# Performance work log

Hardware: AMD Instinct MI355X
Metric: run time of the kernel (lower is better)

The kernel has to match this reference:

```python
import jax, jax.numpy as jnp
import numpy as np

HEADS = 4
DIM_HEAD = 32
EPS = 1e-5


def setup_inputs() -> dict:
    key = jax.random.key(0)
    ks = jax.random.split(key, 3)
    b, c, h, w = 32, 256, 64, 64
    hidden = HEADS * DIM_HEAD  # 128
    x = jax.random.normal(ks[0], (b, c, h, w), dtype=jnp.float32)
    w_qkv = jax.random.normal(ks[1], (3 * hidden, c), dtype=jnp.float32) * 0.02
    w_out = jax.random.normal(ks[2], (c, hidden), dtype=jnp.float32) * 0.02
    b_out = jnp.zeros((c,), dtype=jnp.float32)
    gn_w = jnp.ones((c,), dtype=jnp.float32)
    gn_b = jnp.zeros((c,), dtype=jnp.float32)
    return {"x": x, "w_qkv": w_qkv, "w_out": w_out, "b_out": b_out,
            "gn_w": gn_w, "gn_b": gn_b}


def reference(x, w_qkv, w_out, b_out, gn_w, gn_b):
    b, c, h, w = x.shape
    n = h * w
    scale = DIM_HEAD ** (-0.5)
    # 1x1 conv (no bias) -> qkv, shape (b, 3*hidden, h, w)
    qkv = jnp.einsum('bchw,oc->bohw', x, w_qkv)
    qkv = qkv.reshape(b, 3, HEADS, DIM_HEAD, n)
    q, k, v = qkv[:, 0], qkv[:, 1], qkv[:, 2]  # each (b, H, d, n)
    q = jax.nn.softmax(q, axis=-2) * scale     # softmax over d
    k = jax.nn.softmax(k, axis=-1)             # softmax over n
    # linear attention core
    context = jnp.einsum('bhdn,bhen->bhde', k, v)   # (b, H, d, e)
    out = jnp.einsum('bhde,bhdn->bhen', context, q)  # (b, H, e, n)
    out = out.reshape(b, HEADS * DIM_HEAD, h, w)
    # 1x1 conv with bias
    out = jnp.einsum('bchw,oc->bohw', out, w_out) + b_out[None, :, None, None]
    # GroupNorm(1, dim): normalize over (C, H, W) per sample
    mean = out.mean(axis=(1, 2, 3), keepdims=True)
    var = out.var(axis=(1, 2, 3), keepdims=True)
    out = (out - mean) * jax.lax.rsqrt(var + EPS)
    out = out * gn_w[None, :, None, None] + gn_b[None, :, None, None]
    return out
```

## Files before the change

kernel.cpp:

```cpp
#include <hip/hip_runtime.h>
#include <math.h>

#define B_ 32
#define C_ 256
#define N_ 4096
#define HID_ 128
#define OC3_ 384
#define HEADS_ 4
#define DH_ 32
#define LNM_ (C_*N_)

typedef unsigned short u16;
typedef __attribute__((ext_vector_type(8))) short short8;
typedef __attribute__((ext_vector_type(4))) float f32x4;

__device__ inline u16 f2b(float f) {
  union { float f; unsigned int u; } c; c.f = f;
  unsigned int u = c.u;
  return (u16)((u + 0x7fffu + ((u >> 16) & 1u)) >> 16);
}
__device__ inline float b2f(u16 b) {
  union { float f; unsigned int u; } c; c.u = (unsigned int)b << 16; return c.f;
}
__device__ inline void load_lds16(const u16* g, u16* l) {
  __builtin_amdgcn_global_load_lds(
      (const __attribute__((address_space(1))) void*)g,
      (__attribute__((address_space(3))) void*)l, 16, 0, 0);
}

__global__ void k_cast_w(const float* __restrict__ wq, const float* __restrict__ wo,
                         u16* __restrict__ wqb, u16* __restrict__ wob) {
  int i = blockIdx.x * 256 + threadIdx.x;
  if (i < OC3_ * C_) wqb[i] = f2b(wq[i]);
  if (i < C_ * HID_) wob[i] = f2b(wo[i]);
}

__global__ __launch_bounds__(256) void k_transpose(const float* __restrict__ x,
                                                   u16* __restrict__ xt) {
  int b = blockIdx.z;
  int n0 = blockIdx.x * 64, c0 = blockIdx.y * 64;
  __shared__ float t[64][65];
  const float* xp = x + (size_t)b * C_ * N_;
  u16* xo = xt + (size_t)b * N_ * C_;
  int tid = threadIdx.x;
  int r = tid >> 4, c4 = (tid & 15) * 4;
  #pragma unroll
  for (int i = 0; i < 4; i++) {
    int cl = r + i * 16;
    float4 v = *(const float4*)&xp[(size_t)(c0 + cl) * N_ + n0 + c4];
    t[cl][c4 + 0] = v.x; t[cl][c4 + 1] = v.y; t[cl][c4 + 2] = v.z; t[cl][c4 + 3] = v.w;
  }
  __syncthreads();
  #pragma unroll
  for (int i = 0; i < 4; i++) {
    int nl = r + i * 16;
    ushort4 o;
    o.x = f2b(t[c4 + 0][nl]); o.y = f2b(t[c4 + 1][nl]);
    o.z = f2b(t[c4 + 2][nl]); o.w = f2b(t[c4 + 3][nl]);
    *(ushort4*)&xo[(size_t)(n0 + nl) * C_ + c0 + c4] = o;
  }
}

__global__ void k_zero(float* __restrict__ p, int n) {
  int i = blockIdx.x * blockDim.x + threadIdx.x;
  int stride = gridDim.x * blockDim.x;
  for (; i < n; i += stride) p[i] = 0.f;
}

template<int KDIM, bool OUTBF16>
__global__ __launch_bounds__(256) void k_gemm_mfma(
    const u16* __restrict__ A, const u16* __restrict__ Ball, void* __restrict__ Call,
    const float* __restrict__ bias, float* __restrict__ bsum, int Mtot) {
  int b = blockIdx.z;
  int m0 = blockIdx.y * 128, n0 = blockIdx.x * 128;
  const u16* Bt = Ball + (size_t)b * N_ * KDIM;
  __shared__ __align__(16) u16 As[4096];
  __shared__ __align__(16) u16 Bs[4096];
  __shared__ float red[8];
  int tid = threadIdx.x;
  int w = tid >> 6, l = tid & 63, l16 = l & 15, quad = l >> 4;
  int wm = w & 1, wn = w >> 1;
  f32x4 acc[4][4] = {};

  for (int k0 = 0; k0 < KDIM; k0 += 32) {
    #pragma unroll
    for (int i = 0; i < 2; i++) {
      int chunk = i * 256 + tid;
      int c = chunk >> 7, m = chunk & 127;
      const u16* ga = A  + (size_t)(m0 + m) * KDIM + k0 + c * 8;
      const u16* gb = Bt + (size_t)(n0 + m) * KDIM + k0 + c * 8;
      u16* la = As + (size_t)(i * 256 + (tid & ~63)) * 8;
      u16* lb = Bs + (size_t)(i * 256 + (tid & ~63)) * 8;
      load_lds16(ga, la);
      load_lds16(gb, lb);
    }
    __syncthreads();
    short8 af[4], bf[4];
    #pragma unroll
    for (int mi = 0; mi < 4; mi++)
      af[mi] = *(const short8*)&As[(size_t)(quad * 128 + wm * 64 + mi * 16 + l16) * 8];
    #pragma unroll
    for (int nj = 0; nj < 4; nj++)
      bf[nj] = *(const short8*)&Bs[(size_t)(quad * 128 + wn * 64 + nj * 16 + l16) * 8];
    #pragma unroll
    for (int mi = 0; mi < 4; mi++)
      #pragma unroll
      for (int nj = 0; nj < 4; nj++)
        acc[mi][nj] = __builtin_amdgcn_mfma_f32_16x16x32_bf16(af[mi], bf[nj], acc[mi][nj], 0, 0, 0);
    __syncthreads();
  }

  if constexpr (OUTBF16) {
    u16* Co = (u16*)Call + (size_t)b * Mtot * N_;
    u16* lw = As + w * 1024;
    #pragma unroll
    for (int mi = 0; mi < 4; mi++) {
      #pragma unroll
      for (int nj = 0; nj < 4; nj++)
        #pragma unroll
        for (int r = 0; r < 4; r++)
          lw[(quad * 4 + r) * 64 + nj * 16 + l16] = f2b(acc[mi][nj][r]);
      #pragma unroll
      for (int p = 0; p < 2; p++) {
        int chunk = p * 64 + l;
        int row = chunk >> 3, cc = chunk & 7;
        uint4 v = *(const uint4*)&lw[chunk * 8];
        *(uint4*)&Co[(size_t)(m0 + wm * 64 + mi * 16 + row) * N_ + n0 + wn * 64 + cc * 8] = v;
      }
    }
  } else {
    float* Co = (float*)Call + (size_t)b * Mtot * N_;
    float s1 = 0.f, s2 = 0.f;
    #pragma unroll
    for (int mi = 0; mi < 4; mi++)
      #pragma unroll
      for (int r = 0; r < 4; r++) {
        int m = m0 + wm * 64 + mi * 16 + quad * 4 + r;
        float bv = bias[m];
        #pragma unroll
        for (int nj = 0; nj < 4; nj++) {
          int n = n0 + wn * 64 + nj * 16 + l16;
          float v = acc[mi][nj][r] + bv;
          s1 += v; s2 += v * v;
          Co[(size_t)m * N_ + n] = v;
        }
      }
    #pragma unroll
    for (int o = 32; o; o >>= 1) { s1 += __shfl_xor(s1, o); s2 += __shfl_xor(s2, o); }
    if (l == 0) { red[w] = s1; red[4 + w] = s2; }
    __syncthreads();
    if (tid == 0) {
      atomicAdd(&bsum[2 * b],     red[0] + red[1] + red[2] + red[3]);
      atomicAdd(&bsum[2 * b + 1], red[4] + red[5] + red[6] + red[7]);
    }
  }
}

__global__ __launch_bounds__(256) void k_kstats(const u16* __restrict__ qkvb,
    float* __restrict__ rmax, float* __restrict__ rinv) {
  int r = blockIdx.x;
  int b = r >> 7, rem = r & 127;
  const u16* row = qkvb + (size_t)b * OC3_ * N_ + (size_t)(HID_ + rem) * N_;
  int tid = threadIdx.x;
  float v[16];
  #pragma unroll
  for (int p = 0; p < 2; p++) {
    uint4 u = *(const uint4*)&row[(size_t)(p * 256 + tid) * 8];
    unsigned int uu[4] = {u.x, u.y, u.z, u.w};
    #pragma unroll
    for (int j = 0; j < 4; j++) {
      v[p * 8 + j * 2 + 0] = b2f((u16)(uu[j] & 0xffff));
      v[p * 8 + j * 2 + 1] = b2f((u16)(uu[j] >> 16));
    }
  }
  float m = -1e30f;
  #pragma unroll
  for (int i = 0; i < 16; i++) m = fmaxf(m, v[i]);
  #pragma unroll
  for (int o = 32; o; o >>= 1) m = fmaxf(m, __shfl_xor(m, o));
  __shared__ float sm[4], ss[4];
  int w = tid >> 6;
  if ((tid & 63) == 0) sm[w] = m;
  __syncthreads();
  m = fmaxf(fmaxf(sm[0], sm[1]), fmaxf(sm[2], sm[3]));
  float s = 0.f;
  #pragma unroll
  for (int i = 0; i < 16; i++) s += __expf(v[i] - m);
  #pragma unroll
  for (int o = 32; o; o >>= 1) s += __shfl_xor(s, o);
  if ((tid & 63) == 0) ss[w] = s;
  __syncthreads();
  if (tid == 0) {
    rmax[r] = m;
    rinv[r] = 1.f / (ss[0] + ss[1] + ss[2] + ss[3]);
  }
}

#define CCH 128
__global__ __launch_bounds__(256) void k_context(const u16* __restrict__ qkvb,
    const float* __restrict__ rmax, const float* __restrict__ rinv,
    float* __restrict__ ctx) {
  int bh = blockIdx.y;
  int b = bh >> 2, hd = bh & 3;
  int c0 = blockIdx.x * 4;
  const u16* kb = qkvb + (size_t)b * OC3_ * N_ + (size_t)(HID_ + hd * DH_) * N_;
  const u16* vb = qkvb + (size_t)b * OC3_ * N_ + (size_t)(2 * HID_ + hd * DH_) * N_;
  __shared__ float ks[32][129];
  __shared__ float vs[128][40];
  int tid = threadIdx.x;
  int n8 = (tid & 15) * 8;
  int dd = tid >> 3, e0 = (tid & 7) * 4;
  f32x4 acc = {};
  for (int cc = 0; cc < 4; cc++) {
    int nb = (c0 + cc) * CCH;
    if (cc) __syncthreads();
    #pragma unroll
    for (int h = 0; h < 2; h++) {
      int d = (tid >> 4) + h * 16;
      float rm = rmax[bh * 32 + d], ri = rinv[bh * 32 + d];
      uint4 ku = *(const uint4*)&kb[(size_t)d * N_ + nb + n8];
      uint4 vu = *(const uint4*)&vb[(size_t)d * N_ + nb + n8];
      unsigned int kk[4] = {ku.x, ku.y, ku.z, ku.w};
      unsigned int vv[4] = {vu.x, vu.y, vu.z, vu.w};
      #pragma unroll
      for (int j = 0; j < 4; j++) {
        ks[d][n8 + j * 2 + 0] = __expf(b2f((u16)(kk[j] & 0xffff)) - rm) * ri;
        ks[d][n8 + j * 2 + 1] = __expf(b2f((u16)(kk[j] >> 16)) - rm) * ri;
        vs[n8 + j * 2 + 0][d] = b2f((u16)(vv[j] & 0xffff));
        vs[n8 + j * 2 + 1][d] = b2f((u16)(vv[j] >> 16));
      }
    }
    __syncthreads();
    for (int n = 0; n < CCH; n++) {
      float kd = ks[dd][n];
      f32x4 v4 = *(const f32x4*)&vs[n][e0];
      acc += kd * v4;
    }
  }
  float* cp = &ctx[(size_t)(bh * 32 + dd) * 32 + e0];
  atomicAdd(cp + 0, acc[0]); atomicAdd(cp + 1, acc[1]);
  atomicAdd(cp + 2, acc[2]); atomicAdd(cp + 3, acc[3]);
}

__global__ __launch_bounds__(256) void k_attnout(const u16* __restrict__ qkvb,
    const float* __restrict__ ctx, u16* __restrict__ hidt) {
  int tile = blockIdx.x, bh = blockIdx.y;
  int b = bh >> 2, hd = bh & 3;
  const u16* qbase = qkvb + (size_t)b * OC3_ * N_ + (size_t)(hd * DH_) * N_;
  __shared__ float cs[32][40];
  __shared__ unsigned int hs[256][16];
  int tid = threadIdx.x;
  for (int idx = tid; idx < 1024; idx += 256) {
    int d = idx >> 5, e = idx & 31;
    cs[d][e] = ctx[(size_t)bh * 1024 + idx];
  }
  __syncthreads();
  int n = tile * 256 + tid;
  float q[32];
  float m = -1e30f;
  #pragma unroll
  for (int d = 0; d < 32; d++) { q[d] = b2f(qbase[(size_t)d * N_ + n]); m = fmaxf(m, q[d]); }
  float s = 0.f;
  #pragma unroll
  for (int d = 0; d < 32; d++) { q[d] = __expf(q[d] - m); s += q[d]; }
  float inv = 0.17677669529663687f / s;
  #pragma unroll
  for (int d = 0; d < 32; d++) q[d] *= inv;
  #pragma unroll
  for (int e0 = 0; e0 < 32; e0 += 4) {
    f32x4 a = {};
    #pragma unroll
    for (int d = 0; d < 32; d++) {
      f32x4 c4 = *(const f32x4*)&cs[d][e0];
      a += q[d] * c4;
    }
    hs[tid][e0 / 2 + 0] = (unsigned int)f2b(a[0]) | ((unsigned int)f2b(a[1]) << 16);
    hs[tid][e0 / 2 + 1] = (unsigned int)f2b(a[2]) | ((unsigned int)f2b(a[3]) << 16);
  }
  __syncthreads();
  #pragma unroll
  for (int it = 0; it < 8; it++) {
    int q2 = it * 256 + tid;
    int nl = q2 >> 3, c2 = q2 & 7;
    uint2 v = *(const uint2*)&hs[nl][c2 * 2];
    *(uint2*)&hidt[((size_t)b * N_ + tile * 256 + nl) * HID_ + hd * 32 + c2 * 4] = v;
  }
}

__global__ void k_finalize(float* __restrict__ bsum) {
  int b = threadIdx.x;
  if (b < B_) {
    float s1 = bsum[2 * b], s2 = bsum[2 * b + 1];
    float mean = s1 * (1.f / LNM_);
    float var = s2 * (1.f / LNM_) - mean * mean;
    bsum[2 * b] = mean;
    bsum[2 * b + 1] = rsqrtf(var + 1e-5f);
  }
}

__global__ __launch_bounds__(256) void k_norm(float* __restrict__ out,
    const float* __restrict__ bsum, const float* __restrict__ gnw,
    const float* __restrict__ gnb) {
  size_t v = (size_t)blockIdx.x * 256 + threadIdx.x;
  int c = (int)((v >> 10) & 255);
  int b = (int)(v >> 18);
  float mean = bsum[2 * b], rstd = bsum[2 * b + 1];
  float w = gnw[c] * rstd;
  float sh = gnb[c] - mean * w;
  float4 x = ((const float4*)out)[v];
  x.x = x.x * w + sh; x.y = x.y * w + sh;
  x.z = x.z * w + sh; x.w = x.w * w + sh;
  ((float4*)out)[v] = x;
}

extern "C" void kernel_launch(void* const* d_in, const int* in_sizes, int n_in,
                              void* d_out, int out_size, void* d_ws, size_t ws_size,
                              hipStream_t stream) {
  const float* x     = (const float*)d_in[0];
  const float* w_qkv = (const float*)d_in[1];
  const float* w_out = (const float*)d_in[2];
  const float* b_out = (const float*)d_in[3];
  const float* gn_w  = (const float*)d_in[4];
  const float* gn_b  = (const float*)d_in[5];
  float* out = (float*)d_out;

  u16* qkvb = (u16*)d_ws;
  u16* xt   = qkvb + (size_t)B_ * OC3_ * N_;
  u16* hidt = xt;
  float* ctx  = (float*)(xt + (size_t)B_ * N_ * C_);
  float* bsum = ctx + 131072;
  float* rmax = bsum + 64;
  float* rinv = rmax + 4096;
  u16* wqb = (u16*)(rinv + 4096);
  u16* wob = wqb + OC3_ * C_;

  k_cast_w<<<384, 256, 0, stream>>>(w_qkv, w_out, wqb, wob);
  k_transpose<<<dim3(64, 4, 32), 256, 0, stream>>>(x, xt);
  k_zero<<<64, 256, 0, stream>>>(ctx, 131072 + 64);
  k_gemm_mfma<256, true><<<dim3(32, 3, 32), 256, 0, stream>>>(wqb, xt, qkvb, nullptr, nullptr, OC3_);
  k_kstats<<<4096, 256, 0, stream>>>(qkvb, rmax, rinv);
  k_context<<<dim3(8, 128), 256, 0, stream>>>(qkvb, rmax, rinv, ctx);
  k_attnout<<<dim3(16, 128), 256, 0, stream>>>(qkvb, ctx, hidt);
  k_gemm_mfma<128, false><<<dim3(32, 2, 32), 256, 0, stream>>>(wob, hidt, out, b_out, bsum, C_);
  k_finalize<<<1, 64, 0, stream>>>(bsum);
  k_norm<<<32768, 256, 0, stream>>>(out, bsum, gn_w, gn_b);
}
```

Measured before the change: 487.5 us.

## Compute linear-attention context with bf16 MFMA and partial buffers instead of atomics

Rewrites the context kernel so that softmax-normalised K and V are fed straight from global memory into 16x16x32 bf16 MFMA instructions, replacing the LDS-staged scalar FMA loop. Each block writes its partial context to a separate buffer (4 partitions), and the attention-output kernel sums those partials, which removes the float atomics. The zeroing kernel is dropped and its bsum clearing is folded into the weight-cast kernel. The normalised K is now rounded to bf16, which slightly lowers precision. The context step is a small share of the total runtime.

```diff
diff --git a/kernel.cpp b/kernel.cpp
--- a/kernel.cpp
+++ b/kernel.cpp
@@ -9,6 +9,7 @@
 #define HEADS_ 4
 #define DH_ 32
 #define LNM_ (C_*N_)
+#define CTXP_ 4
 
 typedef unsigned short u16;
 typedef __attribute__((ext_vector_type(8))) short short8;
@@ -29,10 +30,12 @@
 }
 
 __global__ void k_cast_w(const float* __restrict__ wq, const float* __restrict__ wo,
-                         u16* __restrict__ wqb, u16* __restrict__ wob) {
+                         u16* __restrict__ wqb, u16* __restrict__ wob,
+                         float* __restrict__ bsum) {
   int i = blockIdx.x * 256 + threadIdx.x;
   if (i < OC3_ * C_) wqb[i] = f2b(wq[i]);
   if (i < C_ * HID_) wob[i] = f2b(wo[i]);
+  if (i < 64) bsum[i] = 0.f;
 }
 
 __global__ __launch_bounds__(256) void k_transpose(const float* __restrict__ x,
@@ -59,12 +62,6 @@
     o.z = f2b(t[c4 + 2][nl]); o.w = f2b(t[c4 + 3][nl]);
     *(ushort4*)&xo[(size_t)(n0 + nl) * C_ + c0 + c4] = o;
   }
-}
-
-__global__ void k_zero(float* __restrict__ p, int n) {
-  int i = blockIdx.x * blockDim.x + threadIdx.x;
-  int stride = gridDim.x * blockDim.x;
-  for (; i < n; i += stride) p[i] = 0.f;
 }
 
 template<int KDIM, bool OUTBF16>
@@ -196,54 +193,68 @@
   }
 }
 
-#define CCH 128
 __global__ __launch_bounds__(256) void k_context(const u16* __restrict__ qkvb,
     const float* __restrict__ rmax, const float* __restrict__ rinv,
-    float* __restrict__ ctx) {
-  int bh = blockIdx.y;
+    float* __restrict__ ctxp) {
+  int blk = blockIdx.x, bh = blockIdx.y;
   int b = bh >> 2, hd = bh & 3;
-  int c0 = blockIdx.x * 4;
   const u16* kb = qkvb + (size_t)b * OC3_ * N_ + (size_t)(HID_ + hd * DH_) * N_;
   const u16* vb = qkvb + (size_t)b * OC3_ * N_ + (size_t)(2 * HID_ + hd * DH_) * N_;
-  __shared__ float ks[32][129];
-  __shared__ float vs[128][40];
-  int tid = threadIdx.x;
-  int n8 = (tid & 15) * 8;
-  int dd = tid >> 3, e0 = (tid & 7) * 4;
-  f32x4 acc = {};
-  for (int cc = 0; cc < 4; cc++) {
-    int nb = (c0 + cc) * CCH;
-    if (cc) __syncthreads();
-    #pragma unroll
-    for (int h = 0; h < 2; h++) {
-      int d = (tid >> 4) + h * 16;
-      float rm = rmax[bh * 32 + d], ri = rinv[bh * 32 + d];
-      uint4 ku = *(const uint4*)&kb[(size_t)d * N_ + nb + n8];
-      uint4 vu = *(const uint4*)&vb[(size_t)d * N_ + nb + n8];
-      unsigned int kk[4] = {ku.x, ku.y, ku.z, ku.w};
-      unsigned int vv[4] = {vu.x, vu.y, vu.z, vu.w};
+  __shared__ float redl[4096];
+  int tid = threadIdx.x;
+  int w = tid >> 6, l = tid & 63, l16 = l & 15, quad = l >> 4;
+  float rm[2], ri[2];
+  #pragma unroll
+  for (int mi = 0; mi < 2; mi++) {
+    rm[mi] = rmax[bh * 32 + mi * 16 + l16];
+    ri[mi] = rinv[bh * 32 + mi * 16 + l16];
+  }
+  f32x4 acc[2][2] = {};
+  int nbase = blk * 1024 + w * 256 + quad * 8;
+  #pragma unroll
+  for (int kk = 0; kk < 8; kk++) {
+    int n0 = nbase + kk * 32;
+    short8 af[2], bf[2];
+    #pragma unroll
+    for (int nj = 0; nj < 2; nj++)
+      bf[nj] = *(const short8*)&vb[(size_t)(nj * 16 + l16) * N_ + n0];
+    #pragma unroll
+    for (int mi = 0; mi < 2; mi++) {
+      uint4 u = *(const uint4*)&kb[(size_t)(mi * 16 + l16) * N_ + n0];
+      unsigned int uu[4] = {u.x, u.y, u.z, u.w};
+      union { unsigned int u[4]; short8 s; } pk;
       #pragma unroll
       for (int j = 0; j < 4; j++) {
-        ks[d][n8 + j * 2 + 0] = __expf(b2f((u16)(kk[j] & 0xffff)) - rm) * ri;
-        ks[d][n8 + j * 2 + 1] = __expf(b2f((u16)(kk[j] >> 16)) - rm) * ri;
-        vs[n8 + j * 2 + 0][d] = b2f((u16)(vv[j] & 0xffff));
-        vs[n8 + j * 2 + 1][d] = b2f((u16)(vv[j] >> 16));
+        float lo = __expf(b2f((u16)(uu[j] & 0xffff)) - rm[mi]) * ri[mi];
+        float hi = __expf(b2f((u16)(uu[j] >> 16))     - rm[mi]) * ri[mi];
+        pk.u[j] = (unsigned int)f2b(lo) | ((unsigned int)f2b(hi) << 16);
       }
-    }
-    __syncthreads();
-    for (int n = 0; n < CCH; n++) {
-      float kd = ks[dd][n];
-      f32x4 v4 = *(const f32x4*)&vs[n][e0];
-      acc += kd * v4;
-    }
-  }
-  float* cp = &ctx[(size_t)(bh * 32 + dd) * 32 + e0];
-  atomicAdd(cp + 0, acc[0]); atomicAdd(cp + 1, acc[1]);
-  atomicAdd(cp + 2, acc[2]); atomicAdd(cp + 3, acc[3]);
+      af[mi] = pk.s;
+    }
+    #pragma unroll
+    for (int mi = 0; mi < 2; mi++)
+      #pragma unroll
+      for (int nj = 0; nj < 2; nj++)
+        acc[mi][nj] = __builtin_amdgcn_mfma_f32_16x16x32_bf16(af[mi], bf[nj], acc[mi][nj], 0, 0, 0);
+  }
+  #pragma unroll
+  for (int mi = 0; mi < 2; mi++)
+    #pragma unroll
+    for (int nj = 0; nj < 2; nj++)
+      #pragma unroll
+      for (int r = 0; r < 4; r++)
+        redl[w * 1024 + (mi * 16 + quad * 4 + r) * 32 + nj * 16 + l16] = acc[mi][nj][r];
+  __syncthreads();
+  float* cp = ctxp + (size_t)blk * 131072 + (size_t)bh * 1024;
+  #pragma unroll
+  for (int j = 0; j < 4; j++) {
+    int idx = j * 256 + tid;
+    cp[idx] = redl[idx] + redl[1024 + idx] + redl[2048 + idx] + redl[3072 + idx];
+  }
 }
 
 __global__ __launch_bounds__(256) void k_attnout(const u16* __restrict__ qkvb,
-    const float* __restrict__ ctx, u16* __restrict__ hidt) {
+    const float* __restrict__ ctxp, u16* __restrict__ hidt) {
   int tile = blockIdx.x, bh = blockIdx.y;
   int b = bh >> 2, hd = bh & 3;
   const u16* qbase = qkvb + (size_t)b * OC3_ * N_ + (size_t)(hd * DH_) * N_;
@@ -251,8 +262,12 @@
   __shared__ unsigned int hs[256][16];
   int tid = threadIdx.x;
   for (int idx = tid; idx < 1024; idx += 256) {
+    float s = 0.f;
+    #pragma unroll
+    for (int p = 0; p < CTXP_; p++)
+      s += ctxp[(size_t)p * 131072 + (size_t)bh * 1024 + idx];
     int d = idx >> 5, e = idx & 31;
-    cs[d][e] = ctx[(size_t)bh * 1024 + idx];
+    cs[d][e] = s;
   }
   __syncthreads();
   int n = tile * 256 + tid;
@@ -328,18 +343,17 @@
   u16* xt   = qkvb + (size_t)B_ * OC3_ * N_;
   u16* hidt = xt;
   float* ctx  = (float*)(xt + (size_t)B_ * N_ * C_);
-  float* bsum = ctx + 131072;
+  float* bsum = ctx + CTXP_ * 131072;
   float* rmax = bsum + 64;
   float* rinv = rmax + 4096;
   u16* wqb = (u16*)(rinv + 4096);
   u16* wob = wqb + OC3_ * C_;
 
-  k_cast_w<<<384, 256, 0, stream>>>(w_qkv, w_out, wqb, wob);
+  k_cast_w<<<384, 256, 0, stream>>>(w_qkv, w_out, wqb, wob, bsum);
   k_transpose<<<dim3(64, 4, 32), 256, 0, stream>>>(x, xt);
-  k_zero<<<64, 256, 0, stream>>>(ctx, 131072 + 64);
   k_gemm_mfma<256, true><<<dim3(32, 3, 32), 256, 0, stream>>>(wqb, xt, qkvb, nullptr, nullptr, OC3_);
   k_kstats<<<4096, 256, 0, stream>>>(qkvb, rmax, rinv);
-  k_context<<<dim3(8, 128), 256, 0, stream>>>(qkvb, rmax, rinv, ctx);
+  k_context<<<dim3(CTXP_, 128), 256, 0, stream>>>(qkvb, rmax, rinv, ctx);
   k_attnout<<<dim3(16, 128), 256, 0, stream>>>(qkvb, ctx, hidt);
   k_gemm_mfma<128, false><<<dim3(32, 2, 32), 256, 0, stream>>>(wob, hidt, out, b_out, bsum, C_);
   k_finalize<<<1, 64, 0, stream>>>(bsum);
```

Measured after the change: 454.4 us. 1.07x faster.
